# Performance work log

Measured on AMD Instinct MI355X. Metric: run time of the kernel, lower is better.

Reference implementation:

```python
import jax, jax.numpy as jnp
import numpy as np

B, T, IN, H, L = 16, 256, 256, 1024, 4

def setup_inputs() -> dict:
    key = jax.random.key(0)
    ks = jax.random.split(key, 5)
    return {
        "x": jax.random.normal(ks[0], (B, T, IN), jnp.float32),
        # gate axis order: 0=forget, 1=input-perc(sigmoid), 2=input-pot(tanh), 3=output
        "Wh": jax.random.normal(ks[1], (L, 4, H, H), jnp.float32) * 0.1,
        "Wx0": jax.random.normal(ks[2], (4, IN, H), jnp.float32) * 0.1,
        "Wx": jax.random.normal(ks[3], (L - 1, 4, H, H), jnp.float32) * 0.1,
        "b": jax.random.normal(ks[4], (L, 4, H), jnp.float32) * 0.1,
    }

def _run_layer(inp, wh, wx, bias):
    # inp: [B, T, D]; wh: [4, H, H]; wx: [4, D, H]; bias: [4, H]
    # Precompute all input projections for every timestep (time-major for scan).
    pre = jnp.einsum('btd,gdh->tbgh', inp, wx) + bias  # [T, B, 4, H]
    Bn = inp.shape[0]
    Hn = wh.shape[-1]

    def step(carry, px):
        h, c = carry  # short_term, long_term
        g = px + jnp.einsum('bh,gho->bgo', h, wh)  # [B, 4, H]
        f = jax.nn.sigmoid(g[:, 0])       # forget factor
        perc = jax.nn.sigmoid(g[:, 1])    # input gate (percent)
        pot = jnp.tanh(g[:, 2])           # input gate (potential)
        o = jax.nn.sigmoid(g[:, 3])       # output gate (uses OLD short_term)
        c_new = f * c + perc * pot
        h_new = jnp.tanh(c_new) * o
        return (h_new, c_new), h_new

    init = (jnp.zeros((Bn, Hn), inp.dtype), jnp.zeros((Bn, Hn), inp.dtype))
    (h, _), hs = jax.lax.scan(step, init, pre)
    return h, jnp.moveaxis(hs, 0, 1)  # final hidden [B,H], all hiddens [B,T,H]

def reference(x, Wh, Wx0, Wx, b):
    h, seq = _run_layer(x, Wh[0], Wx0, b[0])
    for i in range(1, Wh.shape[0]):
        h, seq = _run_layer(seq, Wh[i], Wx[i - 1], b[i])
    return h  # original returns (final_hidden, None); None dropped
```

## Files before the change

### kernel.cpp

```cpp
#include <hip/hip_runtime.h>


typedef float f32x4 __attribute__((ext_vector_type(4)));
typedef short bf16x8 __attribute__((ext_vector_type(8)));

__device__ __forceinline__ unsigned short f2bf_rn(float x) {
    unsigned int u = __float_as_uint(x);
    u += 0x7FFFu + ((u >> 16) & 1u);
    return (unsigned short)(u >> 16);
}
__device__ __forceinline__ float bf2f(unsigned short s) {
    return __uint_as_float(((unsigned int)s) << 16);
}
__device__ __forceinline__ float sigmoidf_(float x) { return 1.0f / (1.0f + __expf(-x)); }
__device__ __forceinline__ float tanhf_(float x) {
    float e = __expf(2.0f * x);
    return 1.0f - 2.0f / (e + 1.0f);
}

#define MFMA16(a, b, c) __builtin_amdgcn_mfma_f32_16x16x32_bf16((a), (b), (c), 0, 0, 0)

__global__ __launch_bounds__(256)
void pre_gemm(const float* __restrict__ A, const float* __restrict__ W,
              const float* __restrict__ bias, float* __restrict__ out, int K)
{
    __shared__ float As[16][132];
    __shared__ float Bs[16][132];

    const int tid = threadIdx.x;
    const int m0 = blockIdx.y << 7;
    const int n0 = blockIdx.x << 7;
    const int g  = n0 >> 10;
    const int jb = n0 & 1023;
    const float* Wg = W + (size_t)g * K * 1024 + jb;

    const int tx = tid & 15;
    const int ty = tid >> 4;
    const int alk = tid & 15;
    const int alm = tid >> 4;
    const int bln = tid & 127;
    const int blkk = tid >> 7;

    float acc[8][8];
#pragma unroll
    for (int i = 0; i < 8; ++i)
#pragma unroll
        for (int j = 0; j < 8; ++j) acc[i][j] = 0.f;

    for (int k0 = 0; k0 < K; k0 += 16) {
        __syncthreads();
#pragma unroll
        for (int r = 0; r < 8; ++r) {
            int m = alm + (r << 4);
            As[alk][m] = A[(size_t)(m0 + m) * K + (k0 + alk)];
        }
#pragma unroll
        for (int r = 0; r < 8; ++r) {
            int kk = blkk + (r << 1);
            Bs[kk][bln] = Wg[(size_t)(k0 + kk) * 1024 + bln];
        }
        __syncthreads();
#pragma unroll
        for (int k = 0; k < 16; ++k) {
            float a[8], bb[8];
            *(f32x4*)&a[0]  = *(const f32x4*)&As[k][ty << 2];
            *(f32x4*)&a[4]  = *(const f32x4*)&As[k][64 + (ty << 2)];
            *(f32x4*)&bb[0] = *(const f32x4*)&Bs[k][tx << 2];
            *(f32x4*)&bb[4] = *(const f32x4*)&Bs[k][64 + (tx << 2)];
#pragma unroll
            for (int i = 0; i < 8; ++i)
#pragma unroll
                for (int j = 0; j < 8; ++j)
                    acc[i][j] = fmaf(a[i], bb[j], acc[i][j]);
        }
    }

    float bj[8];
#pragma unroll
    for (int j = 0; j < 8; ++j) {
        int nloc = (j < 4) ? ((tx << 2) + j) : (64 + (tx << 2) + (j - 4));
        bj[j] = bias[n0 + nloc];
    }
#pragma unroll
    for (int i = 0; i < 8; ++i) {
        int mloc = (i < 4) ? ((ty << 2) + i) : (64 + (ty << 2) + (i - 4));
        int m = m0 + mloc;
        int bidx = m >> 8;
        int tt   = m & 255;
        float* orow = out + ((size_t)((tt << 4) + bidx) << 12) + n0;
#pragma unroll
        for (int j = 0; j < 8; ++j) {
            int nloc = (j < 4) ? ((tx << 2) + j) : (64 + (tx << 2) + (j - 4));
            orow[nloc] = acc[i][j] + bj[j];
        }
    }
}

__global__ __launch_bounds__(256)
void lstm_scan(const float* __restrict__ pre,
               const float* __restrict__ Wh,
               float* __restrict__ seq_out,
               unsigned short* __restrict__ hhi,
               unsigned short* __restrict__ hlo,
               int* __restrict__ ctr_l1,
               float* __restrict__ final_out,
               int is_last)
{
    const int wg   = blockIdx.x;
    const int tid  = threadIdx.x;
    const int wv   = tid >> 6;
    const int lane = tid & 63;
    const int bc   = lane & 15;
    const int quad = lane >> 4;

    __shared__ float red[4][64][4];
    __shared__ float gsh[16][17];

    const int g   = bc >> 2;
    const int col = (wg << 2) + (bc & 3);
    bf16x8 Whi[8], Wmi[8], Wlo[8];
#pragma unroll
    for (int ck = 0; ck < 8; ++ck) {
#pragma unroll
        for (int j = 0; j < 8; ++j) {
            int k = (wv << 8) + (ck << 5) + (quad << 3) + j;
            float w = Wh[((size_t)g << 20) + ((size_t)k << 10) + col];
            unsigned short hi = f2bf_rn(w);
            float r1 = w - bf2f(hi);
            unsigned short mi = f2bf_rn(r1);
            float r2 = r1 - bf2f(mi);
            unsigned short lo = f2bf_rn(r2);
            Whi[ck][j] = (short)hi;
            Wmi[ck][j] = (short)mi;
            Wlo[ck][j] = (short)lo;
        }
    }

    float creg = 0.f;
    int dead = 0;

    for (int t = 0; t < 256; ++t) {
        float pr[4];
        if (wv == 0) {
            const float* pp = pre + ((size_t)t << 16) + ((size_t)(bc >> 2) << 10)
                              + (wg << 2) + (bc & 3);
#pragma unroll
            for (int r = 0; r < 4; ++r)
                pr[r] = pp[(size_t)((quad << 2) + r) << 12];
        }

        if (t > 0 && wv == 0 && !dead) {
            const int* lb = ctr_l1 + (((t - 1) << 4) << 5);
            bool done = (lane >= 16);
            const int gi5 = (lane & 15) << 5;
            int guard = 0;
            for (;;) {
                if (!done)
                    done = __hip_atomic_load(lb + gi5, __ATOMIC_RELAXED,
                                             __HIP_MEMORY_SCOPE_AGENT) >= 16;
                if (__all(done)) break;
                __builtin_amdgcn_s_sleep(1);
                if (++guard > (1 << 15)) { dead = 1; break; }
            }
        }
        __syncthreads();
        asm volatile("" ::: "memory");

        f32x4 a00 = {0.f, 0.f, 0.f, 0.f};
        f32x4 a01 = a00, a10 = a00, a11 = a00;
        if (t > 0) {
            const size_t pb = ((size_t)(t - 1) << 14) + ((size_t)bc << 10) + (wv << 8);
            const unsigned short* ph = hhi + pb;
            const unsigned short* pl = hlo + pb;
            bf16x8 ahi[8], alo[8];
#pragma unroll
            for (int ck = 0; ck < 8; ++ck) {
                ahi[ck] = *(const bf16x8*)(ph + (ck << 5) + (quad << 3));
                alo[ck] = *(const bf16x8*)(pl + (ck << 5) + (quad << 3));
            }
#pragma unroll
            for (int ck = 0; ck < 8; ++ck) {
                if (ck & 1) {
                    a10 = MFMA16(ahi[ck], Whi[ck], a10);
                    a11 = MFMA16(ahi[ck], Wmi[ck], a11);
                    a10 = MFMA16(ahi[ck], Wlo[ck], a10);
                    a11 = MFMA16(alo[ck], Whi[ck], a11);
                    a10 = MFMA16(alo[ck], Wmi[ck], a10);
                } else {
                    a00 = MFMA16(ahi[ck], Whi[ck], a00);
                    a01 = MFMA16(ahi[ck], Wmi[ck], a01);
                    a00 = MFMA16(ahi[ck], Wlo[ck], a00);
                    a01 = MFMA16(alo[ck], Whi[ck], a01);
                    a00 = MFMA16(alo[ck], Wmi[ck], a00);
                }
            }
        }
        f32x4 acc = (a00 + a01) + (a10 + a11);
        *(f32x4*)&red[wv][lane][0] = acc;
        __syncthreads();

        if (wv == 0) {
            f32x4 s0 = *(const f32x4*)&red[0][lane][0];
            f32x4 s1 = *(const f32x4*)&red[1][lane][0];
            f32x4 s2 = *(const f32x4*)&red[2][lane][0];
            f32x4 s3 = *(const f32x4*)&red[3][lane][0];
            f32x4 s = (s0 + s1) + (s2 + s3);
#pragma unroll
            for (int r = 0; r < 4; ++r)
                gsh[(quad << 2) + r][bc] = s[r] + pr[r];

            const int b2 = lane >> 2, jl2 = lane & 3;
            float fg = sigmoidf_(gsh[b2][jl2]);
            float ig = sigmoidf_(gsh[b2][4 + jl2]);
            float pg = tanhf_(gsh[b2][8 + jl2]);
            float og = sigmoidf_(gsh[b2][12 + jl2]);
            creg = fg * creg + ig * pg;
            float h = tanhf_(creg) * og;

            const int j = (wg << 2) + jl2;
            unsigned short hh = f2bf_rn(h);
            unsigned short hl = f2bf_rn(h - bf2f(hh));
            size_t pidx = ((size_t)t << 14) + ((size_t)b2 << 10) + j;
            __hip_atomic_store(&hhi[pidx], hh, __ATOMIC_RELAXED, __HIP_MEMORY_SCOPE_AGENT);
            __hip_atomic_store(&hlo[pidx], hl, __ATOMIC_RELAXED, __HIP_MEMORY_SCOPE_AGENT);
            if (is_last && t == 255) final_out[((size_t)b2 << 10) + j] = h;

            __builtin_amdgcn_s_waitcnt(0);
            if (lane == 0)
                __hip_atomic_fetch_add(&ctr_l1[((t << 4) + (wg >> 4)) << 5], 1,
                                       __ATOMIC_RELAXED,
                                       __HIP_MEMORY_SCOPE_AGENT);

            if (!is_last)
                seq_out[((size_t)((b2 << 8) + t) << 10) + j] = h;
        }
    }
}

__global__ __launch_bounds__(256)
void lstm_pair(const float* __restrict__ preA,
               const float* __restrict__ WhA,
               const float* __restrict__ WhB,
               const float* __restrict__ WxB,
               const float* __restrict__ biasB,
               float* __restrict__ seq_out,
               unsigned short* __restrict__ hAhi, unsigned short* __restrict__ hAlo,
               unsigned short* __restrict__ hBhi, unsigned short* __restrict__ hBlo,
               int* __restrict__ ctrA,
               int* __restrict__ ctrB,
               float* __restrict__ final_out,
               int is_last)
{
    const int wg   = blockIdx.x;
    const int tid  = threadIdx.x;
    const int wv   = tid >> 6;
    const int lane = tid & 63;
    const int bc   = lane & 15;
    const int quad = lane >> 4;

    __shared__ float red[3][4][64][4];
    __shared__ float gsh[2][16][17];
    __shared__ float ring[2][16][17];

    const int g   = bc >> 2;
    const int col = (wg << 2) + (bc & 3);

    bf16x8 WAh[8], WAm[8], WAl[8];
    bf16x8 WBh[8], WBm[8], WBl[8];
    bf16x8 WXh[8], WXm[8], WXl[8];
#pragma unroll
    for (int ck = 0; ck < 8; ++ck) {
#pragma unroll
        for (int j = 0; j < 8; ++j) {
            const int k = (wv << 8) + (ck << 5) + (quad << 3) + j;
            const size_t widx = ((size_t)g << 20) + ((size_t)k << 10) + col;
            {
                float w = WhA[widx];
                unsigned short hi = f2bf_rn(w); float r1 = w - bf2f(hi);
                unsigned short mi = f2bf_rn(r1); float r2 = r1 - bf2f(mi);
                WAh[ck][j] = (short)hi; WAm[ck][j] = (short)mi;
                WAl[ck][j] = (short)f2bf_rn(r2);
            }
            {
                float w = WhB[widx];
                unsigned short hi = f2bf_rn(w); float r1 = w - bf2f(hi);
                unsigned short mi = f2bf_rn(r1); float r2 = r1 - bf2f(mi);
                WBh[ck][j] = (short)hi; WBm[ck][j] = (short)mi;
                WBl[ck][j] = (short)f2bf_rn(r2);
            }
            {
                float w = WxB[widx];
                unsigned short hi = f2bf_rn(w); float r1 = w - bf2f(hi);
                unsigned short mi = f2bf_rn(r1); float r2 = r1 - bf2f(mi);
                WXh[ck][j] = (short)hi; WXm[ck][j] = (short)mi;
                WXl[ck][j] = (short)f2bf_rn(r2);
            }
        }
    }
    const float biasv = biasB[((size_t)g << 10) + col];

    float creg = 0.f;
    int dead = 0;

    for (int s = 0; s < 258; ++s) {
        float pr[4];
        if (wv == 0 && s < 256) {
            const float* pp = preA + ((size_t)s << 16) + ((size_t)g << 10) + col;
#pragma unroll
            for (int r = 0; r < 4; ++r)
                pr[r] = pp[(size_t)((quad << 2) + r) << 12];
        }

        if (s > 0 && wv == 0 && !dead) {
            bool done;
            const int gi = lane & 15;
            const int* wp;
            if (lane < 16)      { done = (s > 256); wp = ctrA + (((s - 1) << 4) + gi) * 32; }
            else if (lane < 32) { done = (s < 3);   wp = ctrB + (((s - 1) << 4) + gi) * 32; }
            else                { done = true;      wp = ctrA; }
            int guard = 0;
            for (;;) {
                if (!done)
                    done = __hip_atomic_load(wp, __ATOMIC_RELAXED,
                                             __HIP_MEMORY_SCOPE_AGENT) >= 16;
                if (__all(done)) break;
                __builtin_amdgcn_s_sleep(1);
                if (++guard > (1 << 14)) { dead = 1; break; }
            }
        }
        __syncthreads();
        asm volatile("" ::: "memory");

        f32x4 aA0 = {0.f, 0.f, 0.f, 0.f}, aA1 = aA0;
        f32x4 aP0 = aA0, aP1 = aA0;
        f32x4 aB0 = aA0, aB1 = aA0;

        if (s >= 1 && s <= 256) {
            const size_t pb = ((size_t)(s - 1) << 14) + ((size_t)bc << 10) + (wv << 8);
            const unsigned short* ph = hAhi + pb;
            const unsigned short* pl = hAlo + pb;
#pragma unroll
            for (int ck = 0; ck < 8; ++ck) {
                bf16x8 ah = *(const bf16x8*)(ph + (ck << 5) + (quad << 3));
                bf16x8 al = *(const bf16x8*)(pl + (ck << 5) + (quad << 3));
                if (ck & 1) {
                    aA1 = MFMA16(ah, WAh[ck], aA1);
                    aA1 = MFMA16(ah, WAm[ck], aA1);
                    aA1 = MFMA16(ah, WAl[ck], aA1);
                    aA1 = MFMA16(al, WAh[ck], aA1);
                    aA1 = MFMA16(al, WAm[ck], aA1);
                    aP1 = MFMA16(ah, WXh[ck], aP1);
                    aP1 = MFMA16(ah, WXm[ck], aP1);
                    aP1 = MFMA16(ah, WXl[ck], aP1);
                    aP1 = MFMA16(al, WXh[ck], aP1);
                    aP1 = MFMA16(al, WXm[ck], aP1);
                } else {
                    aA0 = MFMA16(ah, WAh[ck], aA0);
                    aA0 = MFMA16(ah, WAm[ck], aA0);
                    aA0 = MFMA16(ah, WAl[ck], aA0);
                    aA0 = MFMA16(al, WAh[ck], aA0);
                    aA0 = MFMA16(al, WAm[ck], aA0);
                    aP0 = MFMA16(ah, WXh[ck], aP0);
                    aP0 = MFMA16(ah, WXm[ck], aP0);
                    aP0 = MFMA16(ah, WXl[ck], aP0);
                    aP0 = MFMA16(al, WXh[ck], aP0);
                    aP0 = MFMA16(al, WXm[ck], aP0);
                }
            }
        }
        if (s >= 3) {
            const size_t pb = ((size_t)(s - 3) << 14) + ((size_t)bc << 10) + (wv << 8);
            const unsigned short* ph = hBhi + pb;
            const unsigned short* pl = hBlo + pb;
#pragma unroll
            for (int ck = 0; ck < 8; ++ck) {
                bf16x8 bh = *(const bf16x8*)(ph + (ck << 5) + (quad << 3));
                bf16x8 bl = *(const bf16x8*)(pl + (ck << 5) + (quad << 3));
                if (ck & 1) {
                    aB1 = MFMA16(bh, WBh[ck], aB1);
                    aB1 = MFMA16(bh, WBm[ck], aB1);
                    aB1 = MFMA16(bh, WBl[ck], aB1);
                    aB1 = MFMA16(bl, WBh[ck], aB1);
                    aB1 = MFMA16(bl, WBm[ck], aB1);
                } else {
                    aB0 = MFMA16(bh, WBh[ck], aB0);
                    aB0 = MFMA16(bh, WBm[ck], aB0);
                    aB0 = MFMA16(bh, WBl[ck], aB0);
                    aB0 = MFMA16(bl, WBh[ck], aB0);
                    aB0 = MFMA16(bl, WBm[ck], aB0);
                }
            }
        }

        *(f32x4*)&red[0][wv][lane][0] = aA0 + aA1;
        *(f32x4*)&red[1][wv][lane][0] = aP0 + aP1;
        *(f32x4*)&red[2][wv][lane][0] = aB0 + aB1;
        __syncthreads();

        if (wv == 0) {
            if (s <= 255) {
                f32x4 s0 = *(const f32x4*)&red[0][0][lane][0];
                f32x4 s1 = *(const f32x4*)&red[0][1][lane][0];
                f32x4 s2 = *(const f32x4*)&red[0][2][lane][0];
                f32x4 s3 = *(const f32x4*)&red[0][3][lane][0];
                f32x4 sm = (s0 + s1) + (s2 + s3);
#pragma unroll
                for (int r = 0; r < 4; ++r)
                    gsh[0][(quad << 2) + r][bc] = sm[r] + pr[r];

                const int b2 = lane >> 2, jl2 = lane & 3;
                float fg = sigmoidf_(gsh[0][b2][jl2]);
                float ig = sigmoidf_(gsh[0][b2][4 + jl2]);
                float pg = tanhf_(gsh[0][b2][8 + jl2]);
                float og = sigmoidf_(gsh[0][b2][12 + jl2]);
                creg = fg * creg + ig * pg;
                float h = tanhf_(creg) * og;
                const int j = (wg << 2) + jl2;
                unsigned short hh = f2bf_rn(h);
                unsigned short hl = f2bf_rn(h - bf2f(hh));
                size_t pidx = ((size_t)s << 14) + ((size_t)b2 << 10) + j;
                __hip_atomic_store(&hAhi[pidx], hh, __ATOMIC_RELAXED, __HIP_MEMORY_SCOPE_AGENT);
                __hip_atomic_store(&hAlo[pidx], hl, __ATOMIC_RELAXED, __HIP_MEMORY_SCOPE_AGENT);
                __builtin_amdgcn_s_waitcnt(0);
                if (lane == 0)
                    __hip_atomic_fetch_add(&ctrA[((s << 4) + (wg >> 4)) << 5], 1,
                                           __ATOMIC_RELAXED,
                                           __HIP_MEMORY_SCOPE_AGENT);
            }
        } else if (wv == 1) {
            if (s >= 2) {
                const int t1 = s - 2;
                f32x4 s0 = *(const f32x4*)&red[2][0][lane][0];
                f32x4 s1 = *(const f32x4*)&red[2][1][lane][0];
                f32x4 s2 = *(const f32x4*)&red[2][2][lane][0];
                f32x4 s3 = *(const f32x4*)&red[2][3][lane][0];
                f32x4 sm = (s0 + s1) + (s2 + s3);
#pragma unroll
                for (int r = 0; r < 4; ++r)
                    gsh[1][(quad << 2) + r][bc] =
                        sm[r] + ring[t1 & 1][(quad << 2) + r][bc];

                const int b2 = lane >> 2, jl2 = lane & 3;
                float fg = sigmoidf_(gsh[1][b2][jl2]);
                float ig = sigmoidf_(gsh[1][b2][4 + jl2]);
                float pg = tanhf_(gsh[1][b2][8 + jl2]);
                float og = sigmoidf_(gsh[1][b2][12 + jl2]);
                creg = fg * creg + ig * pg;
                float h = tanhf_(creg) * og;
                const int j = (wg << 2) + jl2;
                unsigned short hh = f2bf_rn(h);
                unsigned short hl = f2bf_rn(h - bf2f(hh));
                size_t pidx = ((size_t)t1 << 14) + ((size_t)b2 << 10) + j;
                __hip_atomic_store(&hBhi[pidx], hh, __ATOMIC_RELAXED, __HIP_MEMORY_SCOPE_AGENT);
                __hip_atomic_store(&hBlo[pidx], hl, __ATOMIC_RELAXED, __HIP_MEMORY_SCOPE_AGENT);
                __builtin_amdgcn_s_waitcnt(0);
                if (lane == 0)
                    __hip_atomic_fetch_add(&ctrB[((s << 4) + (wg >> 4)) << 5], 1,
                                           __ATOMIC_RELAXED,
                                           __HIP_MEMORY_SCOPE_AGENT);
                if (!is_last)
                    seq_out[((size_t)((b2 << 8) + t1) << 10) + j] = h;
                if (is_last && t1 == 255)
                    final_out[((size_t)b2 << 10) + j] = h;
            }
        } else if (wv == 2) {
            if (s >= 1 && s <= 256) {
                f32x4 q0 = *(const f32x4*)&red[1][0][lane][0];
                f32x4 q1 = *(const f32x4*)&red[1][1][lane][0];
                f32x4 q2 = *(const f32x4*)&red[1][2][lane][0];
                f32x4 q3 = *(const f32x4*)&red[1][3][lane][0];
                f32x4 qm = (q0 + q1) + (q2 + q3);
#pragma unroll
                for (int r = 0; r < 4; ++r)
                    ring[(s - 1) & 1][(quad << 2) + r][bc] = qm[r] + biasv;
            }
        }
    }
}

extern "C" void kernel_launch(void* const* d_in, const int* in_sizes, int n_in,
                              void* d_out, int out_size, void* d_ws, size_t ws_size,
                              hipStream_t stream)
{
    (void)in_sizes; (void)n_in; (void)out_size; (void)ws_size;

    const float* x    = (const float*)d_in[0];
    const float* Wh   = (const float*)d_in[1];
    const float* Wx0  = (const float*)d_in[2];
    const float* Wx   = (const float*)d_in[3];
    const float* bias = (const float*)d_in[4];

    float* pre  = (float*)d_ws;
    float* seqA = pre + 16777216;
    float* reg2 = seqA + 4194304;
    unsigned short* hAhi = (unsigned short*)(reg2 + 4194304);
    unsigned short* hAlo = hAhi + 4194304;
    int* ctr = (int*)(hAlo + 4194304);
    const size_t PAIR_PL = 258 * 16 * 32;
    const size_t FB_PL   = 256 * 16 * 32;

    float* fout = (float*)d_out;
    const dim3 blk(256);
    const dim3 ggrid(32, 32);
    const size_t WLAYER = (size_t)4 * 1024 * 1024;

    int nb = 0;
    if (hipOccupancyMaxActiveBlocksPerMultiprocessor(&nb, lstm_pair, 256, 0)
        != hipSuccess) nb = 0;

    hipMemsetAsync(ctr, 0, 4 * PAIR_PL * sizeof(int), stream);

    if (nb >= 1) {
        unsigned short* hBhi = (unsigned short*)reg2;
        unsigned short* hBlo = hBhi + 4194304;

        pre_gemm<<<ggrid, blk, 0, stream>>>(x, Wx0, bias, pre, 256);
        for (int p01 = 0; p01 < 2; ++p01) {
            const float* p   = pre;
            const float* whA = Wh + (size_t)(2 * p01) * WLAYER;
            const float* whB = Wh + (size_t)(2 * p01 + 1) * WLAYER;
            const float* wxB = Wx + (size_t)(2 * p01) * WLAYER;
            const float* bB  = bias + (size_t)(2 * p01 + 1) * 4096;
            float* so = seqA;
            int* cA = ctr + (size_t)(2 * p01) * PAIR_PL;
            int* cB = cA + PAIR_PL;
            int last = (p01 == 1);
            void* args[] = { (void*)&p, (void*)&whA, (void*)&whB, (void*)&wxB,
                             (void*)&bB, (void*)&so, (void*)&hAhi, (void*)&hAlo,
                             (void*)&hBhi, (void*)&hBlo, (void*)&cA, (void*)&cB,
                             (void*)&fout, (void*)&last };
            hipLaunchCooperativeKernel((void*)lstm_pair, dim3(256), blk, args, 0, stream);
            if (p01 == 0)
                pre_gemm<<<ggrid, blk, 0, stream>>>(seqA, Wx + WLAYER,
                                                    bias + 2 * 4096, pre, 1024);
        }
    } else {
        float* seqB = reg2;
        unsigned short* hhi = hAhi;
        unsigned short* hlo = hAlo;
        for (int l = 0; l < 4; ++l) {
            const float* inp = (l == 0) ? x : ((l & 1) ? seqA : seqB);
            float* outp      = (l & 1) ? seqB : seqA;
            const float* wx  = (l == 0) ? Wx0 : (Wx + (size_t)(l - 1) * WLAYER);
            int K            = (l == 0) ? 256 : 1024;

            pre_gemm<<<ggrid, blk, 0, stream>>>(inp, wx, bias + (size_t)l * 4096, pre, K);

            const float* p = pre;
            const float* wh = Wh + (size_t)l * WLAYER;
            float* so = outp;
            int* pl1 = ctr + (size_t)l * FB_PL;
            int last = (l == 3);
            void* args[] = { (void*)&p, (void*)&wh, (void*)&so, (void*)&hhi,
                             (void*)&hlo, (void*)&pl1, (void*)&fout, (void*)&last };
            hipLaunchCooperativeKernel((void*)lstm_scan, dim3(256), blk, args, 0, stream);
        }
    }
}
```

Baseline: 6.887 ms.

## Split lstm_pair K-reduction across 8 waves with 512-thread blocks

Doubles the lstm_pair workgroup from 4 to 8 waves, so each wave covers 128 instead of 256 of the K dimension in the recurrent matvec. Each wave now holds half as many register-resident bf16 weight splits, which cuts VGPR pressure and halves the per-wave MFMA chain on the serial per-timestep critical path. In exchange, the shared-memory reduction buffer doubles and the gate waves sum 8 partials instead of 4. More waves per block also contend for the same CU's MFMA units.

```diff
diff --git a/kernel.cpp b/kernel.cpp
--- a/kernel.cpp
+++ b/kernel.cpp
@@ -237,7 +237,7 @@
     }
 }
 
-__global__ __launch_bounds__(256)
+__global__ __launch_bounds__(512)
 void lstm_pair(const float* __restrict__ preA,
                const float* __restrict__ WhA,
                const float* __restrict__ WhB,
@@ -258,21 +258,21 @@
     const int bc   = lane & 15;
     const int quad = lane >> 4;
 
-    __shared__ float red[3][4][64][4];
+    __shared__ float red[3][8][64][4];
     __shared__ float gsh[2][16][17];
     __shared__ float ring[2][16][17];
 
     const int g   = bc >> 2;
     const int col = (wg << 2) + (bc & 3);
 
-    bf16x8 WAh[8], WAm[8], WAl[8];
-    bf16x8 WBh[8], WBm[8], WBl[8];
-    bf16x8 WXh[8], WXm[8], WXl[8];
-#pragma unroll
-    for (int ck = 0; ck < 8; ++ck) {
+    bf16x8 WAh[4], WAm[4], WAl[4];
+    bf16x8 WBh[4], WBm[4], WBl[4];
+    bf16x8 WXh[4], WXm[4], WXl[4];
+#pragma unroll
+    for (int ck = 0; ck < 4; ++ck) {
 #pragma unroll
         for (int j = 0; j < 8; ++j) {
-            const int k = (wv << 8) + (ck << 5) + (quad << 3) + j;
+            const int k = (wv << 7) + (ck << 5) + (quad << 3) + j;
             const size_t widx = ((size_t)g << 20) + ((size_t)k << 10) + col;
             {
                 float w = WhA[widx];
@@ -336,11 +336,11 @@
         f32x4 aB0 = aA0, aB1 = aA0;
 
         if (s >= 1 && s <= 256) {
-            const size_t pb = ((size_t)(s - 1) << 14) + ((size_t)bc << 10) + (wv << 8);
+            const size_t pb = ((size_t)(s - 1) << 14) + ((size_t)bc << 10) + (wv << 7);
             const unsigned short* ph = hAhi + pb;
             const unsigned short* pl = hAlo + pb;
 #pragma unroll
-            for (int ck = 0; ck < 8; ++ck) {
+            for (int ck = 0; ck < 4; ++ck) {
                 bf16x8 ah = *(const bf16x8*)(ph + (ck << 5) + (quad << 3));
                 bf16x8 al = *(const bf16x8*)(pl + (ck << 5) + (quad << 3));
                 if (ck & 1) {
@@ -369,11 +369,11 @@
             }
         }
         if (s >= 3) {
-            const size_t pb = ((size_t)(s - 3) << 14) + ((size_t)bc << 10) + (wv << 8);
+            const size_t pb = ((size_t)(s - 3) << 14) + ((size_t)bc << 10) + (wv << 7);
             const unsigned short* ph = hBhi + pb;
             const unsigned short* pl = hBlo + pb;
 #pragma unroll
-            for (int ck = 0; ck < 8; ++ck) {
+            for (int ck = 0; ck < 4; ++ck) {
                 bf16x8 bh = *(const bf16x8*)(ph + (ck << 5) + (quad << 3));
                 bf16x8 bl = *(const bf16x8*)(pl + (ck << 5) + (quad << 3));
                 if (ck & 1) {
@@ -399,11 +399,10 @@
 
         if (wv == 0) {
             if (s <= 255) {
-                f32x4 s0 = *(const f32x4*)&red[0][0][lane][0];
-                f32x4 s1 = *(const f32x4*)&red[0][1][lane][0];
-                f32x4 s2 = *(const f32x4*)&red[0][2][lane][0];
-                f32x4 s3 = *(const f32x4*)&red[0][3][lane][0];
-                f32x4 sm = (s0 + s1) + (s2 + s3);
+                f32x4 sm = {0.f, 0.f, 0.f, 0.f};
+#pragma unroll
+                for (int w = 0; w < 8; ++w)
+                    sm += *(const f32x4*)&red[0][w][lane][0];
 #pragma unroll
                 for (int r = 0; r < 4; ++r)
                     gsh[0][(quad << 2) + r][bc] = sm[r] + pr[r];
@@ -430,11 +429,10 @@
         } else if (wv == 1) {
             if (s >= 2) {
                 const int t1 = s - 2;
-                f32x4 s0 = *(const f32x4*)&red[2][0][lane][0];
-                f32x4 s1 = *(const f32x4*)&red[2][1][lane][0];
-                f32x4 s2 = *(const f32x4*)&red[2][2][lane][0];
-                f32x4 s3 = *(const f32x4*)&red[2][3][lane][0];
-                f32x4 sm = (s0 + s1) + (s2 + s3);
+                f32x4 sm = {0.f, 0.f, 0.f, 0.f};
+#pragma unroll
+                for (int w = 0; w < 8; ++w)
+                    sm += *(const f32x4*)&red[2][w][lane][0];
 #pragma unroll
                 for (int r = 0; r < 4; ++r)
                     gsh[1][(quad << 2) + r][bc] =
@@ -465,11 +463,10 @@
             }
         } else if (wv == 2) {
             if (s >= 1 && s <= 256) {
-                f32x4 q0 = *(const f32x4*)&red[1][0][lane][0];
-                f32x4 q1 = *(const f32x4*)&red[1][1][lane][0];
-                f32x4 q2 = *(const f32x4*)&red[1][2][lane][0];
-                f32x4 q3 = *(const f32x4*)&red[1][3][lane][0];
-                f32x4 qm = (q0 + q1) + (q2 + q3);
+                f32x4 qm = {0.f, 0.f, 0.f, 0.f};
+#pragma unroll
+                for (int w = 0; w < 8; ++w)
+                    qm += *(const f32x4*)&red[1][w][lane][0];
 #pragma unroll
                 for (int r = 0; r < 4; ++r)
                     ring[(s - 1) & 1][(quad << 2) + r][bc] = qm[r] + biasv;
@@ -501,11 +498,12 @@
 
     float* fout = (float*)d_out;
     const dim3 blk(256);
+    const dim3 blkP(512);
     const dim3 ggrid(32, 32);
     const size_t WLAYER = (size_t)4 * 1024 * 1024;
 
     int nb = 0;
-    if (hipOccupancyMaxActiveBlocksPerMultiprocessor(&nb, lstm_pair, 256, 0)
+    if (hipOccupancyMaxActiveBlocksPerMultiprocessor(&nb, lstm_pair, 512, 0)
         != hipSuccess) nb = 0;
 
     hipMemsetAsync(ctr, 0, 4 * PAIR_PL * sizeof(int), stream);
@@ -529,7 +527,7 @@
                              (void*)&bB, (void*)&so, (void*)&hAhi, (void*)&hAlo,
                              (void*)&hBhi, (void*)&hBlo, (void*)&cA, (void*)&cB,
                              (void*)&fout, (void*)&last };
-            hipLaunchCooperativeKernel((void*)lstm_pair, dim3(256), blk, args, 0, stream);
+            hipLaunchCooperativeKernel((void*)lstm_pair, dim3(256), blkP, args, 0, stream);
             if (p01 == 0)
                 pre_gemm<<<ggrid, blk, 0, stream>>>(seqA, Wx + WLAYER,
                                                     bias + 2 * 4096, pre, 1024);
```

After: 6.879 ms. No clear change (-0.1%).
